# Kernel optimization log

Hardware: AMD Instinct MI355X
Metric: run time of the kernel (lower is better)

## Reference

```python
import jax, jax.numpy as jnp
import numpy as np
from jax import lax

D, R, C = 4, 6, 32
P = 2 * R + 1
N = P * P
MR = 12
MP = 2 * MR + 1
MN = MP * MP


def corr_sampler(f_t, f_r, r, dilate):
    # SpatialCorrelationSampler(kernel_size=1, patch_size=2r+1, dilation_patch=dilate)
    # out[b,py,px,y,x] = sum_c f_t[b,c,y,x] * f_r[b,c, y+(py-r)*dilate, x+(px-r)*dilate] (zero pad)
    b, c, h, w = f_t.shape
    p = 2 * r + 1
    pad = r * dilate
    f_r_p = jnp.pad(f_r, ((0, 0), (0, 0), (pad, pad), (pad, pad)))
    offs = jnp.arange(p, dtype=jnp.int32) * dilate
    ii, jj = jnp.meshgrid(offs, offs, indexing='ij')
    shifts = jnp.stack([ii.ravel(), jj.ravel()], 1)  # (p*p, 2)

    def step(_, ij):
        win = lax.dynamic_slice(f_r_p, (0, 0, ij[0], ij[1]), (b, c, h, w))
        return None, jnp.sum(f_t * win, axis=1)  # (b,h,w)

    _, out = lax.scan(step, None, shifts)  # (p*p, b, h, w)
    return out.transpose(1, 0, 2, 3).reshape(b, p, p, h, w)


def bilinear_sample(im, xs, ys):
    # im: (b,c,H,W); xs, ys: (b,h,w) pixel coords; zero padding outside (grid_sample semantics)
    b, c, H, W = im.shape
    x0 = jnp.floor(xs)
    y0 = jnp.floor(ys)
    out = jnp.zeros((b, c) + xs.shape[1:], im.dtype)
    for dy in (0.0, 1.0):
        for dx in (0.0, 1.0):
            xi = x0 + dx
            yi = y0 + dy
            wgt = (1.0 - jnp.abs(xs - xi)) * (1.0 - jnp.abs(ys - yi))
            valid = (xi >= 0) & (xi <= W - 1) & (yi >= 0) & (yi <= H - 1)
            xc = jnp.clip(xi, 0, W - 1).astype(jnp.int32)
            yc = jnp.clip(yi, 0, H - 1).astype(jnp.int32)
            v = jax.vmap(lambda imb, yb, xb: imb[:, yb, xb])(im, yc, xc)  # (b,c,h,w)
            out = out + v * (wgt * valid.astype(im.dtype))[:, None]
    return out


def deform_im2col(im, offset, r):
    # im: (b,c,h,w); offset: (b,h,w,2) with channels (x, y)
    # returns (b, c, (2r+1)^2, h, w), kernel positions row-major over (ky, kx)
    b, c, H, W = im.shape
    h, w = offset.shape[1], offset.shape[2]
    bx = jnp.arange(W, dtype=im.dtype)[None, None, :] + offset[..., 0]  # (b,h,w)
    by = jnp.arange(H, dtype=im.dtype)[None, :, None] + offset[..., 1]
    ks = jnp.arange(-r, r + 1, dtype=im.dtype)
    ky, kx = jnp.meshgrid(ks, ks, indexing='ij')
    koff = jnp.stack([ky.ravel(), kx.ravel()], 1)  # (N, 2) as (ky, kx)

    def step(_, k):
        return None, bilinear_sample(im, bx + k[1], by + k[0])  # (b,c,h,w)

    _, cols = lax.scan(step, None, koff)  # (N,b,c,h,w)
    return cols.transpose(1, 2, 0, 3, 4)


def unfold(x, r):
    # F.unfold(x, kernel_size=2r+1, padding=r) reshaped to (b,c,N,h,w)
    b, c, h, w = x.shape
    p = 2 * r + 1
    xp = jnp.pad(x, ((0, 0), (0, 0), (r, r), (r, r)))
    iy = jnp.arange(p)[:, None] + jnp.arange(h)[None, :]  # (p,h)
    ix = jnp.arange(p)[:, None] + jnp.arange(w)[None, :]  # (p,w)
    win = xp[:, :, iy[:, None, :, None], ix[None, :, None, :]]  # (b,c,p,p,h,w)
    return win.reshape(b, c, p * p, h, w)


def colorizer_forward(feats_r, feats_t, quantized_r, ref_index, current_ind, dil_int):
    ref_list = [int(v) for v in np.asarray(ref_index)]
    nref = feats_r.shape[0]
    gaps = [int(current_ind) - x for x in ref_list]
    nsearch = len([g for g in gaps if g > int(dil_int)])
    dirates = [min(4, g // int(dil_int) + 1) for g in gaps if g > int(dil_int)]
    b, c, h, w = feats_t.shape

    gy, gx = jnp.meshgrid(jnp.arange(-MR, MR + 1, dtype=feats_t.dtype),
                          jnp.arange(-MR, MR + 1, dtype=feats_t.dtype), indexing='ij')
    grid = jnp.stack([gx, gy], -1).reshape(1, MP, MP, 1, 1, 2)

    corrs = []
    offset0 = None
    for i in range(nsearch):
        cc = corr_sampler(feats_t, feats_r[i], MR, dirates[i])  # (b,MP,MP,h,w)
        cc = jax.nn.softmax(cc.reshape(b, MN, h * w), axis=1)
        cc = cc.reshape(b, MP, MP, h, w, 1)
        # expected displacement (x, y); NOTE: original code keeps only the LAST offset0
        offset0 = (cc * grid).sum(axis=(1, 2)) * dirates[i]  # (b,h,w,2)
        col0 = deform_im2col(feats_r[i], offset0, R)  # (b,c,N,h,w)
        corr = (feats_t[:, :, None] * col0).sum(axis=1).reshape(b, N, h * w)
        corrs.append(corr)
    for i in range(nsearch, nref):
        cr = corr_sampler(feats_t, feats_r[i], R, 1).reshape(b, N, h * w)
        corrs.append(cr)

    corr = jax.nn.softmax(jnp.concatenate(corrs, 1), axis=1)[:, None]  # (b,1,nref*N,hw)

    qr = [quantized_r[i][:, :, ::D, ::D] for i in range(nref)]  # prep: stride D (C!=1)
    cols = [deform_im2col(qr[i], offset0, R).reshape(b, C, N, h * w) for i in range(nsearch)]
    cols += [unfold(qr[i], R).reshape(b, C, N, h * w) for i in range(nsearch, nref)]
    image_uf = jnp.concatenate(cols, 2)  # (b,C,nref*N,hw)

    out = (corr * image_uf).sum(axis=2).reshape(b, C, h, w)
    return out


def setup_inputs() -> dict:
    key = jax.random.key(0)
    k1, k2, k3 = jax.random.split(key, 3)
    feats_r = jax.random.normal(k1, (3, 2, 64, 48, 48), jnp.float32) * 0.1
    feats_t = jax.random.normal(k2, (2, 64, 48, 48), jnp.float32) * 0.1
    quantized_r = jax.random.normal(k3, (3, 2, 32, 192, 192), jnp.float32)
    ref_index = np.array([0, 20, 35], dtype=np.int64)
    return {"feats_r": feats_r, "feats_t": feats_t, "quantized_r": quantized_r,
            "ref_index": ref_index, "current_ind": 40, "dil_int": 15}


def reference(feats_r, feats_t, quantized_r, ref_index, current_ind, dil_int):
    return colorizer_forward(feats_r, feats_t, quantized_r, ref_index, current_ind, dil_int)
```

## Files before the change

### kernel.cpp

```cpp
#include <hip/hip_runtime.h>


typedef unsigned short ushort_t;
typedef unsigned int uint_t;
typedef __attribute__((ext_vector_type(8))) short short8;
typedef __attribute__((ext_vector_type(4))) float f32x4;

namespace {
constexpr int NPIX = 2304;
constexpr int FC   = 64;
constexpr int QC   = 32;

constexpr size_t OFS_FTB  = 0;
constexpr size_t OFS_FRB  = OFS_FTB + (size_t)2*NPIX*FC*2;
constexpr size_t OFS_QRCL = OFS_FRB + (size_t)6*NPIX*FC*2;
constexpr size_t OFS_ACC  = OFS_QRCL + (size_t)6*NPIX*QC*4;
constexpr size_t OFS_CORB = OFS_ACC + (size_t)4*5*NPIX*3*4;
}

__device__ __forceinline__ float blockMax(float v, float* scr) {
  #pragma unroll
  for (int o = 32; o > 0; o >>= 1) v = fmaxf(v, __shfl_down(v, o));
  const int wid = threadIdx.x >> 6;
  __syncthreads();
  if ((threadIdx.x & 63) == 0) scr[wid] = v;
  __syncthreads();
  float r = fmaxf(fmaxf(scr[0], scr[1]), fmaxf(scr[2], scr[3]));
  __syncthreads();
  return r;
}

__device__ __forceinline__ float blockSum(float v, float* scr) {
  #pragma unroll
  for (int o = 32; o > 0; o >>= 1) v += __shfl_down(v, o);
  const int wid = threadIdx.x >> 6;
  __syncthreads();
  if ((threadIdx.x & 63) == 0) scr[wid] = v;
  __syncthreads();
  float r = scr[0] + scr[1] + scr[2] + scr[3];
  __syncthreads();
  return r;
}

__device__ __forceinline__ ushort_t f2b(float f) {
  uint_t u = __float_as_uint(f);
  return (ushort_t)((u + 0x7fffu + ((u >> 16) & 1u)) >> 16);
}

__global__ void zero_kernel(float4* p, int n4) {
  int i = blockIdx.x * 256 + threadIdx.x;
  if (i < n4) p[i] = float4{0.f, 0.f, 0.f, 0.f};
}

__global__ __launch_bounds__(256) void pack_feats(const float* __restrict__ ft,
                                                  const float* __restrict__ fr,
                                                  ushort_t* __restrict__ ftb,
                                                  ushort_t* __restrict__ frb) {
  __shared__ float lds[64][65];
  const int mat = blockIdx.y;
  const int p0  = blockIdx.x * 64;
  const float* src = (mat < 2) ? (ft + (size_t)mat * FC * NPIX)
                               : (fr + (size_t)(mat - 2) * FC * NPIX);
  ushort_t* dst = (mat < 2) ? (ftb + (size_t)mat * NPIX * FC)
                            : (frb + (size_t)(mat - 2) * NPIX * FC);
  const int lane = threadIdx.x & 63, row = threadIdx.x >> 6;
  #pragma unroll
  for (int ch = row; ch < 64; ch += 4)
    lds[ch][lane] = src[(size_t)ch * NPIX + p0 + lane];
  __syncthreads();
  #pragma unroll
  for (int p = row; p < 64; p += 4)
    dst[(size_t)(p0 + p) * FC + lane] = f2b(lds[lane][p]);
}

__global__ __launch_bounds__(256) void pack_qr(const float* __restrict__ q,
                                               float* __restrict__ qrcl) {
  const int idx = blockIdx.x * 256 + threadIdx.x;
  if (idx >= 6 * NPIX * QC) return;
  const int ch = idx & 31;
  int rest = idx >> 5;
  const int x = rest % 48; rest /= 48;
  const int y = rest % 48; rest /= 48;
  const int ib = rest;
  qrcl[idx] = q[(size_t)(ib * 32 + ch) * 36864 + (size_t)(4 * y) * 192 + 4 * x];
}

__global__ __launch_bounds__(64) void gram_kernel(const ushort_t* __restrict__ ftb,
                                                  const ushort_t* __restrict__ frb,
                                                  float* __restrict__ accb,
                                                  float* __restrict__ corb) {
  const int y  = blockIdx.x;
  const int m0 = blockIdx.y * 16;
  int mode, b, chunk, c0, c1;
  if (blockIdx.z < 20) {
    mode = blockIdx.z / 10;
    const int rem = blockIdx.z % 10;
    b = rem / 5; chunk = rem % 5;
    c0 = chunk * 5; c1 = c0 + 5;
  } else {
    const int zz = blockIdx.z - 20;
    mode = 2; b = zz / 3; chunk = zz % 3;
    c0 = (chunk == 0) ? 0 : (chunk == 1) ? 5 : 9;
    c1 = (chunk == 0) ? 5 : (chunk == 1) ? 9 : 13;
  }
  const int d   = (mode == 0) ? 3 : (mode == 1) ? 2 : 1;
  const int RAD = (mode == 2) ? 6 : 12;

  const int lane = threadIdx.x;
  const int col  = lane & 15;
  const int kg   = lane >> 4;

  const short8* ftv = (const short8*)(ftb + ((size_t)b * NPIX + y * 48 + m0 + col) * FC);
  short8 aF0 = ftv[kg];
  short8 aF1 = ftv[4 + kg];

  float wm[3][4], dxv[3][4];
  int sbase[3][4];
  #pragma unroll
  for (int nt = 0; nt < 3; ++nt) {
    #pragma unroll
    for (int r = 0; r < 4; ++r) {
      const int xr   = m0 + kg * 4 + r;
      const int diff = nt * 16 + col - xr;
      const int q    = diff / d;
      const bool v   = (diff % d == 0) && (q >= -RAD) && (q <= RAD);
      wm[nt][r]  = v ? 1.f : 0.f;
      dxv[nt][r] = (float)q;
      sbase[nt][r] = ((int)b * NPIX + y * 48 + xr) * 169 + (q + 6);
    }
  }

  const ushort_t* frmat = frb + (size_t)(mode * 2 + b) * NPIX * FC;
  float se[4] = {0,0,0,0}, sx[4] = {0,0,0,0}, sy[4] = {0,0,0,0};

  for (int dy = c0; dy < c1; ++dy) {
    const int yy = y + (dy - RAD) * d;
    if (yy < 0 || yy >= 48) continue;
    const float dyv = (float)(dy - RAD);
    const short8* frow = (const short8*)(frmat + (size_t)yy * 48 * FC);
    #pragma unroll
    for (int nt = 0; nt < 3; ++nt) {
      const short8* bp = frow + (size_t)(nt * 16 + col) * 8;
      short8 b0 = bp[kg], b1 = bp[4 + kg];
      f32x4 c = {0.f, 0.f, 0.f, 0.f};
      c = __builtin_amdgcn_mfma_f32_16x16x32_bf16(aF0, b0, c, 0, 0, 0);
      c = __builtin_amdgcn_mfma_f32_16x16x32_bf16(aF1, b1, c, 0, 0, 0);
      if (mode < 2) {
        #pragma unroll
        for (int r = 0; r < 4; ++r) {
          const float e = __expf(c[r]) * wm[nt][r];
          se[r] += e;
          sx[r] = fmaf(e, dxv[nt][r], sx[r]);
          sy[r] = fmaf(e, dyv, sy[r]);
        }
      } else {
        #pragma unroll
        for (int r = 0; r < 4; ++r)
          if (wm[nt][r] != 0.f) corb[sbase[nt][r] + dy * 13] = c[r];
      }
    }
  }

  if (mode < 2) {
    #pragma unroll
    for (int r = 0; r < 4; ++r) {
      #pragma unroll
      for (int m = 1; m <= 8; m <<= 1) {
        se[r] += __shfl_xor(se[r], m);
        sx[r] += __shfl_xor(sx[r], m);
        sy[r] += __shfl_xor(sy[r], m);
      }
    }
    if (col == 0) {
      #pragma unroll
      for (int r = 0; r < 4; ++r) {
        float* a = accb + ((((size_t)(mode * 2 + b) * 5 + chunk) * NPIX)
                           + y * 48 + m0 + kg * 4 + r) * 3;
        a[0] = se[r]; a[1] = sx[r]; a[2] = sy[r];
      }
    }
  }
}

__global__ __launch_bounds__(256) void fuse_kernel(const ushort_t* __restrict__ ftb,
                                                   const ushort_t* __restrict__ frb,
                                                   const float* __restrict__ accb,
                                                   const float* __restrict__ corb,
                                                   const float* __restrict__ qrcl,
                                                   float* __restrict__ out) {
  const int pix = blockIdx.x, b = blockIdx.y;
  const int x = pix % 48, y = pix / 48;
  const int tid = threadIdx.x;
  __shared__ float sD[2][208];
  __shared__ float sp[507];
  __shared__ float soff[4];
  __shared__ float scr[4];
  __shared__ float red[8][33];
  __shared__ int   gaddr[196];
  __shared__ float gw0[196], gw1[196];
  __shared__ int   gaddr2[169];

  if (tid < 2) {
    const int d = (tid == 0) ? 3 : 2;
    const float* a = accb + (((size_t)(tid * 2 + b) * 5) * NPIX + pix) * 3;
    float se = 0.f, sx = 0.f, sy = 0.f;
    #pragma unroll
    for (int c = 0; c < 5; ++c) {
      se += a[(size_t)c * NPIX * 3 + 0];
      sx += a[(size_t)c * NPIX * 3 + 1];
      sy += a[(size_t)c * NPIX * 3 + 2];
    }
    const int klox = max(-12, -(x / d)), khix = min(12, (47 - x) / d);
    const int kloy = max(-12, -(y / d)), khiy = min(12, (47 - y) / d);
    const int nvx = khix - klox + 1, nvy = khiy - kloy + 1;
    const int svx = (klox + khix) * nvx / 2, svy = (kloy + khiy) * nvy / 2;
    se += (float)(625 - nvx * nvy);
    sx -= (float)(nvy * svx);
    sy -= (float)(nvx * svy);
    soff[tid * 2 + 0] = (float)d * sx / se;
    soff[tid * 2 + 1] = (float)d * sy / se;
  }
  __syncthreads();

  int bx0a[2], by0a[2];
  float fxa[2], fya[2];
  #pragma unroll
  for (int rr = 0; rr < 2; ++rr) {
    const float bxf = floorf((float)x + soff[rr * 2]);
    const float byf = floorf((float)y + soff[rr * 2 + 1]);
    fxa[rr] = (float)x + soff[rr * 2] - bxf;
    fya[rr] = (float)y + soff[rr * 2 + 1] - byf;
    bx0a[rr] = (int)bxf - 6;
    by0a[rr] = (int)byf - 6;
  }

  {
    const int lane = tid & 63, wv = tid >> 6;
    const int arow = lane & 15, kg = lane >> 4;
    const short8* ftv = (const short8*)(ftb + ((size_t)b * NPIX + pix) * FC);
    const short8 bF0 = ftv[kg], bF1 = ftv[4 + kg];
    for (int gi = wv; gi < 26; gi += 4) {
      const int rr = gi / 13, grp = gi % 13;
      const int g = grp * 16 + arow;
      short8 a0 = {0,0,0,0,0,0,0,0}, a1 = {0,0,0,0,0,0,0,0};
      if (g < 196) {
        const int gy = by0a[rr] + g / 14, gx = bx0a[rr] + g % 14;
        if (gy >= 0 && gy < 48 && gx >= 0 && gx < 48) {
          const short8* fp = (const short8*)(frb + ((size_t)(rr * 2 + b) * NPIX + gy * 48 + gx) * FC);
          a0 = fp[kg]; a1 = fp[4 + kg];
        }
      }
      f32x4 c = {0.f, 0.f, 0.f, 0.f};
      c = __builtin_amdgcn_mfma_f32_16x16x32_bf16(a0, bF0, c, 0, 0, 0);
      c = __builtin_amdgcn_mfma_f32_16x16x32_bf16(a1, bF1, c, 0, 0, 0);
      if (arow == 0)
        *(f32x4*)&sD[rr][grp * 16 + kg * 4] = c;
    }
  }
  __syncthreads();

  float lmax = -1e30f;
  for (int s = tid; s < 507; s += 256) {
    float v;
    if (s < 338) {
      const int rr = s / 169, n = s % 169;
      const float fx = fxa[rr], fy = fya[rr];
      const float w00 = (1.f - fy) * (1.f - fx), w01 = (1.f - fy) * fx;
      const float w10 = fy * (1.f - fx),        w11 = fy * fx;
      const int a_ = n / 13, c2 = n % 13;
      const float* Dp = sD[rr];
      v = w00 * Dp[a_ * 14 + c2]       + w01 * Dp[a_ * 14 + c2 + 1]
        + w10 * Dp[(a_ + 1) * 14 + c2] + w11 * Dp[(a_ + 1) * 14 + c2 + 1];
    } else {
      v = corb[((size_t)b * NPIX + pix) * 169 + (s - 338)];
    }
    sp[s] = v; lmax = fmaxf(lmax, v);
  }
  lmax = blockMax(lmax, scr);
  float ls = 0.f;
  for (int s = tid; s < 507; s += 256) { const float e = __expf(sp[s] - lmax); sp[s] = e; ls += e; }
  ls = blockSum(ls, scr);
  const float inv = 1.f / ls;
  for (int s = tid; s < 507; s += 256) sp[s] *= inv;
  __syncthreads();

  const float fx = fxa[1], fy = fya[1];
  const int bx0 = bx0a[1], by0 = by0a[1];
  if (tid < 196) {
    const int ty = tid / 14, tx = tid % 14;
    const float w00 = (1.f - fy) * (1.f - fx), w01 = (1.f - fy) * fx;
    const float w10 = fy * (1.f - fx),        w11 = fy * fx;
    auto P = [&](const float* base, int a, int c2) -> float {
      return (a >= 0 && a < 13 && c2 >= 0 && c2 < 13) ? base[a * 13 + c2] : 0.f;
    };
    const float s0 = w00 * P(sp, ty, tx)     + w01 * P(sp, ty, tx - 1)
                   + w10 * P(sp, ty - 1, tx) + w11 * P(sp, ty - 1, tx - 1);
    const float s1 = w00 * P(sp + 169, ty, tx)     + w01 * P(sp + 169, ty, tx - 1)
                   + w10 * P(sp + 169, ty - 1, tx) + w11 * P(sp + 169, ty - 1, tx - 1);
    const int gy = by0 + ty, gx = bx0 + tx;
    const bool v = (gy >= 0 && gy < 48 && gx >= 0 && gx < 48);
    gaddr[tid] = v ? (gy * 48 + gx) * QC : 0;
    gw0[tid] = v ? s0 : 0.f;
    gw1[tid] = v ? s1 : 0.f;
  }
  if (tid < 169) {
    const int yy = y + tid / 13 - 6, xx = x + tid % 13 - 6;
    const bool v = (yy >= 0 && yy < 48 && xx >= 0 && xx < 48);
    gaddr2[tid] = v ? (yy * 48 + xx) * QC : 0;
    if (!v) sp[338 + tid] = 0.f;
  }
  __syncthreads();

  const int ch = tid & 31, g8 = tid >> 5;
  const float* q0 = qrcl + (size_t)(0 + b) * NPIX * QC;
  const float* q1 = qrcl + (size_t)(2 + b) * NPIX * QC;
  const float* q2 = qrcl + (size_t)(4 + b) * NPIX * QC;
  float acc = 0.f;
  for (int s = g8; s < 196; s += 8) {
    const int a = gaddr[s];
    acc = fmaf(gw0[s], q0[a + ch], acc);
    acc = fmaf(gw1[s], q1[a + ch], acc);
  }
  for (int s = g8; s < 169; s += 8)
    acc = fmaf(sp[338 + s], q2[gaddr2[s] + ch], acc);
  red[g8][ch] = acc;
  __syncthreads();
  if (g8 == 0) {
    float t = 0.f;
    #pragma unroll
    for (int k = 0; k < 8; ++k) t += red[k][ch];
    out[((size_t)(b * 32 + ch) * 48 + y) * 48 + x] = t;
  }
}

extern "C" void kernel_launch(void* const* d_in, const int* in_sizes, int n_in,
                              void* d_out, int out_size, void* d_ws, size_t ws_size,
                              hipStream_t stream) {
  (void)in_sizes; (void)n_in; (void)out_size; (void)ws_size;
  const float* feats_r     = (const float*)d_in[0];
  const float* feats_t     = (const float*)d_in[1];
  const float* quantized_r = (const float*)d_in[2];
  char* ws = (char*)d_ws;
  ushort_t* ftb  = (ushort_t*)(ws + OFS_FTB);
  ushort_t* frb  = (ushort_t*)(ws + OFS_FRB);
  float*    qrcl = (float*)(ws + OFS_QRCL);
  float*    accb = (float*)(ws + OFS_ACC);
  float*    corb = (float*)(ws + OFS_CORB);

  const int corb_n4 = (2 * NPIX * 169) / 4;
  zero_kernel<<<(corb_n4 + 255) / 256, 256, 0, stream>>>((float4*)corb, corb_n4);
  pack_feats<<<dim3(36, 8), 256, 0, stream>>>(feats_t, feats_r, ftb, frb);
  pack_qr<<<(6 * NPIX * QC + 255) / 256, 256, 0, stream>>>(quantized_r, qrcl);
  gram_kernel<<<dim3(48, 3, 26), 64, 0, stream>>>(ftb, frb, accb, corb);
  fuse_kernel<<<dim3(NPIX, 2), 256, 0, stream>>>(ftb, frb, accb, corb, qrcl, (float*)d_out);
}
```

Measured before the change: 164.8 us.

## Merge pack kernels, drop zero pass, template gram modes, skip softmax max

Combines the feature and quantized-ref packing into one launch, with the qr gather staged through LDS for coalesced writes. The corr-buffer zeroing kernel is removed by masking out-of-range entries at read time. The gram kernel is templated per mode so branches and divisions resolve at compile time. Per-chunk partial sums are laid out contiguously per pixel and read as float4. In the fuse kernel the softmax max pass and the normalisation pass are dropped, with the final output scaled by the inverse sum instead. Omitting the max subtraction risks overflow if correlations are large.

```diff
diff --git a/kernel.cpp b/kernel.cpp
--- a/kernel.cpp
+++ b/kernel.cpp
@@ -15,19 +15,7 @@
 constexpr size_t OFS_FRB  = OFS_FTB + (size_t)2*NPIX*FC*2;
 constexpr size_t OFS_QRCL = OFS_FRB + (size_t)6*NPIX*FC*2;
 constexpr size_t OFS_ACC  = OFS_QRCL + (size_t)6*NPIX*QC*4;
-constexpr size_t OFS_CORB = OFS_ACC + (size_t)4*5*NPIX*3*4;
-}
-
-__device__ __forceinline__ float blockMax(float v, float* scr) {
-  #pragma unroll
-  for (int o = 32; o > 0; o >>= 1) v = fmaxf(v, __shfl_down(v, o));
-  const int wid = threadIdx.x >> 6;
-  __syncthreads();
-  if ((threadIdx.x & 63) == 0) scr[wid] = v;
-  __syncthreads();
-  float r = fmaxf(fmaxf(scr[0], scr[1]), fmaxf(scr[2], scr[3]));
-  __syncthreads();
-  return r;
+constexpr size_t OFS_CORB = OFS_ACC + (size_t)4*NPIX*16*4;
 }
 
 __device__ __forceinline__ float blockSum(float v, float* scr) {
@@ -47,64 +35,60 @@
   return (ushort_t)((u + 0x7fffu + ((u >> 16) & 1u)) >> 16);
 }
 
-__global__ void zero_kernel(float4* p, int n4) {
-  int i = blockIdx.x * 256 + threadIdx.x;
-  if (i < n4) p[i] = float4{0.f, 0.f, 0.f, 0.f};
-}
-
-__global__ __launch_bounds__(256) void pack_feats(const float* __restrict__ ft,
-                                                  const float* __restrict__ fr,
-                                                  ushort_t* __restrict__ ftb,
-                                                  ushort_t* __restrict__ frb) {
-  __shared__ float lds[64][65];
-  const int mat = blockIdx.y;
-  const int p0  = blockIdx.x * 64;
-  const float* src = (mat < 2) ? (ft + (size_t)mat * FC * NPIX)
-                               : (fr + (size_t)(mat - 2) * FC * NPIX);
-  ushort_t* dst = (mat < 2) ? (ftb + (size_t)mat * NPIX * FC)
-                            : (frb + (size_t)(mat - 2) * NPIX * FC);
-  const int lane = threadIdx.x & 63, row = threadIdx.x >> 6;
-  #pragma unroll
-  for (int ch = row; ch < 64; ch += 4)
-    lds[ch][lane] = src[(size_t)ch * NPIX + p0 + lane];
-  __syncthreads();
-  #pragma unroll
-  for (int p = row; p < 64; p += 4)
-    dst[(size_t)(p0 + p) * FC + lane] = f2b(lds[lane][p]);
-}
-
-__global__ __launch_bounds__(256) void pack_qr(const float* __restrict__ q,
-                                               float* __restrict__ qrcl) {
-  const int idx = blockIdx.x * 256 + threadIdx.x;
-  if (idx >= 6 * NPIX * QC) return;
-  const int ch = idx & 31;
-  int rest = idx >> 5;
-  const int x = rest % 48; rest /= 48;
-  const int y = rest % 48; rest /= 48;
-  const int ib = rest;
-  qrcl[idx] = q[(size_t)(ib * 32 + ch) * 36864 + (size_t)(4 * y) * 192 + 4 * x];
-}
-
-__global__ __launch_bounds__(64) void gram_kernel(const ushort_t* __restrict__ ftb,
-                                                  const ushort_t* __restrict__ frb,
-                                                  float* __restrict__ accb,
-                                                  float* __restrict__ corb) {
-  const int y  = blockIdx.x;
-  const int m0 = blockIdx.y * 16;
-  int mode, b, chunk, c0, c1;
-  if (blockIdx.z < 20) {
-    mode = blockIdx.z / 10;
-    const int rem = blockIdx.z % 10;
-    b = rem / 5; chunk = rem % 5;
-    c0 = chunk * 5; c1 = c0 + 5;
+__global__ __launch_bounds__(256) void pack_all(const float* __restrict__ ft,
+                                                const float* __restrict__ fr,
+                                                const float* __restrict__ q,
+                                                ushort_t* __restrict__ ftb,
+                                                ushort_t* __restrict__ frb,
+                                                float* __restrict__ qrcl) {
+  const int bid = blockIdx.x;
+  const int tid = threadIdx.x;
+  if (bid < 288) {
+    __shared__ float lds[64][65];
+    const int mat = bid / 36;
+    const int p0  = (bid % 36) * 64;
+    const float* src = (mat < 2) ? (ft + (size_t)mat * FC * NPIX)
+                                 : (fr + (size_t)(mat - 2) * FC * NPIX);
+    ushort_t* dst = (mat < 2) ? (ftb + (size_t)mat * NPIX * FC)
+                              : (frb + (size_t)(mat - 2) * NPIX * FC);
+    const int lane = tid & 63, row = tid >> 6;
+    #pragma unroll
+    for (int ch = row; ch < 64; ch += 4)
+      lds[ch][lane] = src[(size_t)ch * NPIX + p0 + lane];
+    __syncthreads();
+    #pragma unroll
+    for (int p = row; p < 64; p += 4)
+      dst[(size_t)(p0 + p) * FC + lane] = f2b(lds[lane][p]);
   } else {
-    const int zz = blockIdx.z - 20;
-    mode = 2; b = zz / 3; chunk = zz % 3;
-    c0 = (chunk == 0) ? 0 : (chunk == 1) ? 5 : 9;
-    c1 = (chunk == 0) ? 5 : (chunk == 1) ? 9 : 13;
-  }
-  const int d   = (mode == 0) ? 3 : (mode == 1) ? 2 : 1;
-  const int RAD = (mode == 2) ? 6 : 12;
+    __shared__ float lq[32][49];
+    const int zz = bid - 288;
+    const int ib = zz / 48, yy = zz % 48;
+    const float* src = q + (size_t)ib * 32 * 36864 + (size_t)(4 * yy) * 192;
+    #pragma unroll
+    for (int k = 0; k < 6; ++k) {
+      const int l = tid + k * 256;
+      const int ch = l / 48, xx = l % 48;
+      lq[ch][xx] = src[(size_t)ch * 36864 + 4 * xx];
+    }
+    __syncthreads();
+    float* dst = qrcl + ((size_t)ib * NPIX + yy * 48) * QC;
+    #pragma unroll
+    for (int k = 0; k < 6; ++k) {
+      const int o = tid + k * 256;
+      dst[o] = lq[o & 31][o >> 5];
+    }
+  }
+}
+
+template<int MODE>
+__device__ __forceinline__ void gram_body(const ushort_t* __restrict__ ftb,
+                                          const ushort_t* __restrict__ frb,
+                                          float* __restrict__ accb,
+                                          float* __restrict__ corb,
+                                          int y, int m0, int b, int chunk,
+                                          int c0, int c1) {
+  constexpr int D_  = (MODE == 0) ? 3 : (MODE == 1) ? 2 : 1;
+  constexpr int RAD = (MODE == 2) ? 6 : 12;
 
   const int lane = threadIdx.x;
   const int col  = lane & 15;
@@ -122,22 +106,22 @@
     for (int r = 0; r < 4; ++r) {
       const int xr   = m0 + kg * 4 + r;
       const int diff = nt * 16 + col - xr;
-      const int q    = diff / d;
-      const bool v   = (diff % d == 0) && (q >= -RAD) && (q <= RAD);
+      const int qd   = diff / D_;
+      const bool v   = (diff % D_ == 0) && (qd >= -RAD) && (qd <= RAD);
       wm[nt][r]  = v ? 1.f : 0.f;
-      dxv[nt][r] = (float)q;
-      sbase[nt][r] = ((int)b * NPIX + y * 48 + xr) * 169 + (q + 6);
-    }
-  }
-
-  const ushort_t* frmat = frb + (size_t)(mode * 2 + b) * NPIX * FC;
+      dxv[nt][r] = (float)qd;
+      if (MODE == 2) sbase[nt][r] = ((int)b * NPIX + y * 48 + xr) * 169 + (qd + 6);
+    }
+  }
+
+  const ushort_t* frmat = frb + (size_t)(MODE * 2 + b) * NPIX * FC;
   float se[4] = {0,0,0,0}, sx[4] = {0,0,0,0}, sy[4] = {0,0,0,0};
 
   for (int dy = c0; dy < c1; ++dy) {
-    const int yy = y + (dy - RAD) * d;
-    if (yy < 0 || yy >= 48) continue;
+    const int yyr = y + (dy - RAD) * D_;
+    if (yyr < 0 || yyr >= 48) continue;
     const float dyv = (float)(dy - RAD);
-    const short8* frow = (const short8*)(frmat + (size_t)yy * 48 * FC);
+    const short8* frow = (const short8*)(frmat + (size_t)yyr * 48 * FC);
     #pragma unroll
     for (int nt = 0; nt < 3; ++nt) {
       const short8* bp = frow + (size_t)(nt * 16 + col) * 8;
@@ -145,7 +129,7 @@
       f32x4 c = {0.f, 0.f, 0.f, 0.f};
       c = __builtin_amdgcn_mfma_f32_16x16x32_bf16(aF0, b0, c, 0, 0, 0);
       c = __builtin_amdgcn_mfma_f32_16x16x32_bf16(aF1, b1, c, 0, 0, 0);
-      if (mode < 2) {
+      if (MODE < 2) {
         #pragma unroll
         for (int r = 0; r < 4; ++r) {
           const float e = __expf(c[r]) * wm[nt][r];
@@ -161,7 +145,7 @@
     }
   }
 
-  if (mode < 2) {
+  if (MODE < 2) {
     #pragma unroll
     for (int r = 0; r < 4; ++r) {
       #pragma unroll
@@ -174,11 +158,34 @@
     if (col == 0) {
       #pragma unroll
       for (int r = 0; r < 4; ++r) {
-        float* a = accb + ((((size_t)(mode * 2 + b) * 5 + chunk) * NPIX)
-                           + y * 48 + m0 + kg * 4 + r) * 3;
+        const int p = y * 48 + m0 + kg * 4 + r;
+        float* a = accb + ((size_t)(MODE * 2 + b) * NPIX + p) * 16 + chunk * 3;
         a[0] = se[r]; a[1] = sx[r]; a[2] = sy[r];
       }
     }
+  }
+}
+
+__global__ __launch_bounds__(64) void gram_kernel(const ushort_t* __restrict__ ftb,
+                                                  const ushort_t* __restrict__ frb,
+                                                  float* __restrict__ accb,
+                                                  float* __restrict__ corb) {
+  const int y  = blockIdx.x;
+  const int m0 = blockIdx.y * 16;
+  const int z  = blockIdx.z;
+  if (z < 10) {
+    const int b = z / 5, chunk = z % 5;
+    gram_body<0>(ftb, frb, accb, corb, y, m0, b, chunk, chunk * 5, chunk * 5 + 5);
+  } else if (z < 20) {
+    const int zz = z - 10;
+    const int b = zz / 5, chunk = zz % 5;
+    gram_body<1>(ftb, frb, accb, corb, y, m0, b, chunk, chunk * 5, chunk * 5 + 5);
+  } else {
+    const int zz = z - 20;
+    const int b = zz / 3, chunk = zz % 3;
+    const int c0 = (chunk == 0) ? 0 : (chunk == 1) ? 5 : 9;
+    const int c1 = (chunk == 0) ? 5 : (chunk == 1) ? 9 : 13;
+    gram_body<2>(ftb, frb, accb, corb, y, m0, b, chunk, c0, c1);
   }
 }
 
@@ -191,7 +198,7 @@
   const int pix = blockIdx.x, b = blockIdx.y;
   const int x = pix % 48, y = pix / 48;
   const int tid = threadIdx.x;
-  __shared__ float sD[2][208];
+  __shared__ __align__(16) float sD[2][208];
   __shared__ float sp[507];
   __shared__ float soff[4];
   __shared__ float scr[4];
@@ -202,14 +209,13 @@
 
   if (tid < 2) {
     const int d = (tid == 0) ? 3 : 2;
-    const float* a = accb + (((size_t)(tid * 2 + b) * 5) * NPIX + pix) * 3;
-    float se = 0.f, sx = 0.f, sy = 0.f;
-    #pragma unroll
-    for (int c = 0; c < 5; ++c) {
-      se += a[(size_t)c * NPIX * 3 + 0];
-      sx += a[(size_t)c * NPIX * 3 + 1];
-      sy += a[(size_t)c * NPIX * 3 + 2];
-    }
+    const float4* a4 = (const float4*)(accb + ((size_t)(tid * 2 + b) * NPIX + pix) * 16);
+    float t[16];
+    *(float4*)&t[0]  = a4[0]; *(float4*)&t[4]  = a4[1];
+    *(float4*)&t[8]  = a4[2]; *(float4*)&t[12] = a4[3];
+    float se = t[0] + t[3] + t[6] + t[9] + t[12];
+    float sx = t[1] + t[4] + t[7] + t[10] + t[13];
+    float sy = t[2] + t[5] + t[8] + t[11] + t[14];
     const int klox = max(-12, -(x / d)), khix = min(12, (47 - x) / d);
     const int kloy = max(-12, -(y / d)), khiy = min(12, (47 - y) / d);
     const int nvx = khix - klox + 1, nvy = khiy - kloy + 1;
@@ -222,17 +228,12 @@
   }
   __syncthreads();
 
-  int bx0a[2], by0a[2];
-  float fxa[2], fya[2];
-  #pragma unroll
-  for (int rr = 0; rr < 2; ++rr) {
-    const float bxf = floorf((float)x + soff[rr * 2]);
-    const float byf = floorf((float)y + soff[rr * 2 + 1]);
-    fxa[rr] = (float)x + soff[rr * 2] - bxf;
-    fya[rr] = (float)y + soff[rr * 2 + 1] - byf;
-    bx0a[rr] = (int)bxf - 6;
-    by0a[rr] = (int)byf - 6;
-  }
+  const float bxf0 = floorf((float)x + soff[0]), byf0 = floorf((float)y + soff[1]);
+  const float bxf1 = floorf((float)x + soff[2]), byf1 = floorf((float)y + soff[3]);
+  const float fx0 = (float)x + soff[0] - bxf0, fy0 = (float)y + soff[1] - byf0;
+  const float fx1 = (float)x + soff[2] - bxf1, fy1 = (float)y + soff[3] - byf1;
+  const int bx00 = (int)bxf0 - 6, by00 = (int)byf0 - 6;
+  const int bx01 = (int)bxf1 - 6, by01 = (int)byf1 - 6;
 
   {
     const int lane = tid & 63, wv = tid >> 6;
@@ -240,13 +241,15 @@
     const short8* ftv = (const short8*)(ftb + ((size_t)b * NPIX + pix) * FC);
     const short8 bF0 = ftv[kg], bF1 = ftv[4 + kg];
     for (int gi = wv; gi < 26; gi += 4) {
-      const int rr = gi / 13, grp = gi % 13;
+      const bool r1 = (gi >= 13);
+      const int grp = r1 ? gi - 13 : gi;
       const int g = grp * 16 + arow;
       short8 a0 = {0,0,0,0,0,0,0,0}, a1 = {0,0,0,0,0,0,0,0};
       if (g < 196) {
-        const int gy = by0a[rr] + g / 14, gx = bx0a[rr] + g % 14;
+        const int gy = (r1 ? by01 : by00) + g / 14;
+        const int gx = (r1 ? bx01 : bx00) + g % 14;
         if (gy >= 0 && gy < 48 && gx >= 0 && gx < 48) {
-          const short8* fp = (const short8*)(frb + ((size_t)(rr * 2 + b) * NPIX + gy * 48 + gx) * FC);
+          const short8* fp = (const short8*)(frb + ((size_t)((r1 ? 2 : 0) + b) * NPIX + gy * 48 + gx) * FC);
           a0 = fp[kg]; a1 = fp[4 + kg];
         }
       }
@@ -254,42 +257,40 @@
       c = __builtin_amdgcn_mfma_f32_16x16x32_bf16(a0, bF0, c, 0, 0, 0);
       c = __builtin_amdgcn_mfma_f32_16x16x32_bf16(a1, bF1, c, 0, 0, 0);
       if (arow == 0)
-        *(f32x4*)&sD[rr][grp * 16 + kg * 4] = c;
-    }
-  }
-  __syncthreads();
-
-  float lmax = -1e30f;
+        *(f32x4*)&sD[r1 ? 1 : 0][grp * 16 + kg * 4] = c;
+    }
+  }
+  __syncthreads();
+
+  float ls = 0.f;
   for (int s = tid; s < 507; s += 256) {
     float v;
     if (s < 338) {
-      const int rr = s / 169, n = s % 169;
-      const float fx = fxa[rr], fy = fya[rr];
+      const bool r1 = (s >= 169);
+      const int n = r1 ? s - 169 : s;
+      const float fx = r1 ? fx1 : fx0, fy = r1 ? fy1 : fy0;
       const float w00 = (1.f - fy) * (1.f - fx), w01 = (1.f - fy) * fx;
       const float w10 = fy * (1.f - fx),        w11 = fy * fx;
       const int a_ = n / 13, c2 = n % 13;
-      const float* Dp = sD[rr];
+      const float* Dp = r1 ? sD[1] : sD[0];
       v = w00 * Dp[a_ * 14 + c2]       + w01 * Dp[a_ * 14 + c2 + 1]
         + w10 * Dp[(a_ + 1) * 14 + c2] + w11 * Dp[(a_ + 1) * 14 + c2 + 1];
     } else {
-      v = corb[((size_t)b * NPIX + pix) * 169 + (s - 338)];
-    }
-    sp[s] = v; lmax = fmaxf(lmax, v);
-  }
-  lmax = blockMax(lmax, scr);
-  float ls = 0.f;
-  for (int s = tid; s < 507; s += 256) { const float e = __expf(sp[s] - lmax); sp[s] = e; ls += e; }
+      const int n = s - 338;
+      const int yy = y + n / 13 - 6, xx = x + n % 13 - 6;
+      v = (yy >= 0 && yy < 48 && xx >= 0 && xx < 48)
+            ? corb[((size_t)b * NPIX + pix) * 169 + n] : 0.f;
+    }
+    const float e = __expf(v);
+    sp[s] = e; ls += e;
+  }
   ls = blockSum(ls, scr);
   const float inv = 1.f / ls;
-  for (int s = tid; s < 507; s += 256) sp[s] *= inv;
-  __syncthreads();
-
-  const float fx = fxa[1], fy = fya[1];
-  const int bx0 = bx0a[1], by0 = by0a[1];
+
   if (tid < 196) {
     const int ty = tid / 14, tx = tid % 14;
-    const float w00 = (1.f - fy) * (1.f - fx), w01 = (1.f - fy) * fx;
-    const float w10 = fy * (1.f - fx),        w11 = fy * fx;
+    const float w00 = (1.f - fy1) * (1.f - fx1), w01 = (1.f - fy1) * fx1;
+    const float w10 = fy1 * (1.f - fx1),        w11 = fy1 * fx1;
     auto P = [&](const float* base, int a, int c2) -> float {
       return (a >= 0 && a < 13 && c2 >= 0 && c2 < 13) ? base[a * 13 + c2] : 0.f;
     };
@@ -297,7 +298,7 @@
                    + w10 * P(sp, ty - 1, tx) + w11 * P(sp, ty - 1, tx - 1);
     const float s1 = w00 * P(sp + 169, ty, tx)     + w01 * P(sp + 169, ty, tx - 1)
                    + w10 * P(sp + 169, ty - 1, tx) + w11 * P(sp + 169, ty - 1, tx - 1);
-    const int gy = by0 + ty, gx = bx0 + tx;
+    const int gy = by01 + ty, gx = bx01 + tx;
     const bool v = (gy >= 0 && gy < 48 && gx >= 0 && gx < 48);
     gaddr[tid] = v ? (gy * 48 + gx) * QC : 0;
     gw0[tid] = v ? s0 : 0.f;
@@ -329,7 +330,7 @@
     float t = 0.f;
     #pragma unroll
     for (int k = 0; k < 8; ++k) t += red[k][ch];
-    out[((size_t)(b * 32 + ch) * 48 + y) * 48 + x] = t;
+    out[((size_t)(b * 32 + ch) * 48 + y) * 48 + x] = t * inv;
   }
 }
 
@@ -347,10 +348,7 @@
   float*    accb = (float*)(ws + OFS_ACC);
   float*    corb = (float*)(ws + OFS_CORB);
 
-  const int corb_n4 = (2 * NPIX * 169) / 4;
-  zero_kernel<<<(corb_n4 + 255) / 256, 256, 0, stream>>>((float4*)corb, corb_n4);
-  pack_feats<<<dim3(36, 8), 256, 0, stream>>>(feats_t, feats_r, ftb, frb);
-  pack_qr<<<(6 * NPIX * QC + 255) / 256, 256, 0, stream>>>(quantized_r, qrcl);
+  pack_all<<<576, 256, 0, stream>>>(feats_t, feats_r, quantized_r, ftb, frb, qrcl);
   gram_kernel<<<dim3(48, 3, 26), 64, 0, stream>>>(ftb, frb, accb, corb);
   fuse_kernel<<<dim3(NPIX, 2), 256, 0, stream>>>(ftb, frb, accb, corb, qrcl, (float*)d_out);
 }
```

New measurement: 157.3 us. 1.05x faster.
